# Kernel tuning notes

Measured on AMD Instinct MI355X. Metric: run time of the kernel, lower is better.

The kernel has to match this reference:

```python
import jax, jax.numpy as jnp
import numpy as np

N = 50000      # nodes
E = 800000     # edges (before self-loops)
F_IN = 128     # raw node feature dim
D = 500        # GCN_in_dim = gcn_dim = h_mlp_dim
T = 200000     # number of triplets


def setup_inputs() -> dict:
    key = jax.random.key(0)
    ks = jax.random.split(key, 13)
    s = 0.05
    return {
        "feats": jax.random.normal(ks[0], (N, F_IN), jnp.float32),
        "W_aff": jax.random.normal(ks[1], (F_IN, D), jnp.float32) * s,
        "b_aff": jax.random.normal(ks[2], (D,), jnp.float32) * s,
        "W_gcn": jax.random.normal(ks[3], (D, D), jnp.float32) * s,
        "b_gcn": jax.random.normal(ks[4], (D,), jnp.float32) * s,
        "W_pred_in": jax.random.normal(ks[5], (2 * D, D), jnp.float32) * s,
        "b_pred_in": jax.random.normal(ks[6], (D,), jnp.float32) * s,
        "W_pred_out": jax.random.normal(ks[7], (D, 1), jnp.float32) * s,
        "b_pred_out": jax.random.normal(ks[8], (1,), jnp.float32) * s,
        "src": jax.random.randint(ks[9], (E,), 0, N),
        "dst": jax.random.randint(ks[10], (E,), 0, N),
        "triplets": jax.random.randint(ks[11], (T, 3), 0, N),
    }


def reference(feats, W_aff, b_aff, W_gcn, b_gcn, W_pred_in, b_pred_in,
              W_pred_out, b_pred_out, src, dst, triplets):
    n = feats.shape[0]
    # LinearAffine (use_pre_linearAffine=True)
    x = feats @ W_aff + b_aff                      # [N, D]

    # dgl.add_self_loop
    loop = jnp.arange(n)
    s_idx = jnp.concatenate([src, loop])
    d_idx = jnp.concatenate([dst, loop])

    # GraphConv, norm='both', no edge weights, activation=None
    ones = jnp.ones(s_idx.shape[0], jnp.float32)
    out_deg = jax.ops.segment_sum(ones, s_idx, num_segments=n)
    in_deg = jax.ops.segment_sum(ones, d_idx, num_segments=n)
    norm_src = jnp.where(out_deg > 0, jax.lax.rsqrt(out_deg), 0.0)  # [N]
    norm_dst = jnp.where(in_deg > 0, jax.lax.rsqrt(in_deg), 0.0)    # [N]

    xw = x @ W_gcn                                  # [N, D]
    msg = xw[s_idx] * norm_src[s_idx, None]         # [E+N, D] gather
    agg = jax.ops.segment_sum(msg, d_idx, num_segments=n)  # scatter-add
    embedding = agg * norm_dst[:, None] + b_gcn     # [N, D]

    # triplet gather + MLP_edge_predictor (layer_num=2: cat->Linear->Linear)
    s_feat = embedding[triplets[:, 0]]              # [T, D]
    o_feat = embedding[triplets[:, 2]]              # [T, D]
    t = jnp.concatenate([s_feat, o_feat], axis=-1) @ W_pred_in + b_pred_in
    weights = t @ W_pred_out + b_pred_out           # [T, 1]
    return (weights, embedding)
```

## Files before the change

kernel.cpp:

```cpp
#include <hip/hip_runtime.h>


typedef float f32x4 __attribute__((ext_vector_type(4)));
typedef short s16x8 __attribute__((ext_vector_type(8)));

__device__ __forceinline__ unsigned short f2bf(float f) {
    unsigned u = __float_as_uint(f);
    unsigned r = (u + 0x7FFFu + ((u >> 16) & 1u)) >> 16;
    return (unsigned short)r;
}

__device__ __forceinline__ void async_ld16(const void* g, void* lds) {
    __builtin_amdgcn_global_load_lds(
        (const __attribute__((address_space(1))) unsigned int*)g,
        (__attribute__((address_space(3))) unsigned int*)lds,
        16, 0, 0);
}

__global__ __launch_bounds__(256) void hist2_kernel(
    const int* __restrict__ src, const int* __restrict__ dst,
    int* __restrict__ bhist_src, int* __restrict__ bhist_dst, int E) {
    __shared__ int lhs[256], lhd[256];
    lhs[threadIdx.x] = 0;
    lhd[threadIdx.x] = 0;
    __syncthreads();
    const int stride = gridDim.x * blockDim.x;
    for (int e = blockIdx.x * blockDim.x + threadIdx.x; e < E; e += stride) {
        atomicAdd(&lhs[src[e] >> 8], 1);
        atomicAdd(&lhd[dst[e] >> 8], 1);
    }
    __syncthreads();
    int cs = lhs[threadIdx.x], cd = lhd[threadIdx.x];
    if (cs > 0) atomicAdd(&bhist_src[threadIdx.x], cs);
    if (cd > 0) atomicAdd(&bhist_dst[threadIdx.x], cd);
}

__global__ void bscan2_kernel(const int* __restrict__ bhist_src, const int* __restrict__ bhist_dst,
                              int* __restrict__ sbbase, int* __restrict__ sbcursor,
                              int* __restrict__ dbbase, int* __restrict__ dbcursor,
                              int nbuk, int E) {
    __shared__ int sv[256];
    const int tid = threadIdx.x;

    int c = (tid < nbuk) ? bhist_src[tid] : 0;
    sv[tid] = c;
    __syncthreads();
    for (int st = 1; st < 256; st <<= 1) {
        int t = (tid >= st) ? sv[tid - st] : 0;
        __syncthreads();
        sv[tid] += t;
        __syncthreads();
    }
    if (tid < nbuk) { int ex = sv[tid] - c; sbbase[tid] = ex; sbcursor[tid] = ex; }
    if (tid == 0) sbbase[nbuk] = E;
    __syncthreads();

    c = (tid < nbuk) ? bhist_dst[tid] : 0;
    sv[tid] = c;
    __syncthreads();
    for (int st = 1; st < 256; st <<= 1) {
        int t = (tid >= st) ? sv[tid - st] : 0;
        __syncthreads();
        sv[tid] += t;
        __syncthreads();
    }
    if (tid < nbuk) { int ex = sv[tid] - c; dbbase[tid] = ex; dbcursor[tid] = ex; }
    if (tid == 0) dbbase[nbuk] = E;
}

#define PCH 4096
__global__ __launch_bounds__(256) void partition_kernel(
    const int* __restrict__ src, const int* __restrict__ dst,
    int* __restrict__ bcursor, unsigned long long* __restrict__ pairs,
    int E, int nbuk) {
    __shared__ int lhist[256];
    __shared__ int lbase[256];
    __shared__ int gbase[256];
    __shared__ int scanv[256];
    __shared__ unsigned long long lpair[PCH];
    __shared__ unsigned char lbid[PCH];

    const int tid = threadIdx.x;
    const int c0 = blockIdx.x * PCH;
    int cnt = E - c0; if (cnt > PCH) cnt = PCH;

    lhist[tid] = 0;
    __syncthreads();

    int dv[16], sv[16], rk[16];
#pragma unroll
    for (int q = 0; q < 16; ++q) {
        int e = c0 + q * 256 + tid;
        if (e < E) {
            int d = dst[e];
            dv[q] = d;
            sv[q] = src[e];
            rk[q] = atomicAdd(&lhist[d >> 8], 1);
        } else {
            dv[q] = -1;
        }
    }
    __syncthreads();

    int c = lhist[tid];
    scanv[tid] = c;
    __syncthreads();
    for (int st = 1; st < 256; st <<= 1) {
        int t = (tid >= st) ? scanv[tid - st] : 0;
        __syncthreads();
        scanv[tid] += t;
        __syncthreads();
    }
    lbase[tid] = scanv[tid] - c;
    if (tid < nbuk && c > 0) gbase[tid] = atomicAdd(&bcursor[tid], c);
    __syncthreads();

#pragma unroll
    for (int q = 0; q < 16; ++q) {
        if (dv[q] >= 0) {
            int b = dv[q] >> 8;
            int slot = lbase[b] + rk[q];
            lpair[slot] = ((unsigned long long)(unsigned)dv[q] << 32) | (unsigned)sv[q];
            lbid[slot] = (unsigned char)b;
        }
    }
    __syncthreads();

    for (int i = tid; i < cnt; i += 256) {
        int b = lbid[i];
        pairs[(long)gbase[b] + (i - lbase[b])] = lpair[i];
    }
}

__global__ __launch_bounds__(256) void partition_src_kernel(
    const int* __restrict__ src, int* __restrict__ bcursor,
    int* __restrict__ ssorted, int E, int nbuk) {
    __shared__ int lhist[256];
    __shared__ int lbase[256];
    __shared__ int gbase[256];
    __shared__ int scanv[256];
    __shared__ int lval[PCH];
    __shared__ unsigned char lbid[PCH];

    const int tid = threadIdx.x;
    const int c0 = blockIdx.x * PCH;
    int cnt = E - c0; if (cnt > PCH) cnt = PCH;

    lhist[tid] = 0;
    __syncthreads();

    int sv[16], rk[16];
#pragma unroll
    for (int q = 0; q < 16; ++q) {
        int e = c0 + q * 256 + tid;
        if (e < E) {
            int s = src[e];
            sv[q] = s;
            rk[q] = atomicAdd(&lhist[s >> 8], 1);
        } else {
            sv[q] = -1;
        }
    }
    __syncthreads();

    int c = lhist[tid];
    scanv[tid] = c;
    __syncthreads();
    for (int st = 1; st < 256; st <<= 1) {
        int t = (tid >= st) ? scanv[tid - st] : 0;
        __syncthreads();
        scanv[tid] += t;
        __syncthreads();
    }
    lbase[tid] = scanv[tid] - c;
    if (tid < nbuk && c > 0) gbase[tid] = atomicAdd(&bcursor[tid], c);
    __syncthreads();

#pragma unroll
    for (int q = 0; q < 16; ++q) {
        if (sv[q] >= 0) {
            int b = sv[q] >> 8;
            int slot = lbase[b] + rk[q];
            lval[slot] = sv[q];
            lbid[slot] = (unsigned char)b;
        }
    }
    __syncthreads();

    for (int i = tid; i < cnt; i += 256) {
        int b = lbid[i];
        ssorted[(long)gbase[b] + (i - lbase[b])] = lval[i];
    }
}

__global__ __launch_bounds__(256) void bucket_csr_kernel(
    const unsigned long long* __restrict__ pairs, const int* __restrict__ bbase,
    int* __restrict__ row_ptr, float* __restrict__ ndv,
    int* __restrict__ csr_src, int N) {
    __shared__ int hist[256];
    __shared__ int scanv[256];
    __shared__ int lcur[256];
    const int tid = threadIdx.x;
    const int b = blockIdx.x;
    const int e0 = bbase[b], e1 = bbase[b + 1];

    hist[tid] = 0;
    __syncthreads();
    for (int e = e0 + tid; e < e1; e += 256) {
        int d = (int)(pairs[e] >> 32);
        atomicAdd(&hist[d & 255], 1);
    }
    __syncthreads();

    int c = hist[tid];
    scanv[tid] = c;
    __syncthreads();
    for (int st = 1; st < 256; st <<= 1) {
        int t = (tid >= st) ? scanv[tid - st] : 0;
        __syncthreads();
        scanv[tid] += t;
        __syncthreads();
    }
    int excl = scanv[tid] - c;
    int node = b * 256 + tid;
    if (node < N) {
        row_ptr[node] = e0 + excl;
        ndv[node] = rsqrtf((float)(c + 1));
    }
    if (node == N) row_ptr[N] = e0 + excl;
    lcur[tid] = excl;
    __syncthreads();

    for (int e = e0 + tid; e < e1; e += 256) {
        unsigned long long pr = pairs[e];
        int d = (int)(pr >> 32);
        int r = atomicAdd(&lcur[d & 255], 1);
        csr_src[e0 + r] = (int)(pr & 0xFFFFFFFFu);
    }
}

__global__ __launch_bounds__(256) void bucket_ns_kernel(
    const int* __restrict__ ssorted, const int* __restrict__ sbbase,
    float* __restrict__ ns, int N) {
    __shared__ int hist[256];
    const int tid = threadIdx.x;
    const int b = blockIdx.x;
    const int e0 = sbbase[b], e1 = sbbase[b + 1];
    hist[tid] = 0;
    __syncthreads();
    for (int e = e0 + tid; e < e1; e += 256) atomicAdd(&hist[ssorted[e] & 255], 1);
    __syncthreads();
    int node = b * 256 + tid;
    if (node < N) ns[node] = rsqrtf((float)(hist[tid] + 1));
}

__global__ __launch_bounds__(256) void bcomb_part_kernel(
    const float* __restrict__ b_aff, const float* __restrict__ W_gcn,
    float* __restrict__ part, int D, int PD) {
    int n = blockIdx.x * blockDim.x + threadIdx.x;
    int c = blockIdx.y;
    if (n >= PD) return;
    float s = 0.f;
    if (n < D) {
        int k0 = c * 8;
        int k1 = k0 + 8; if (k1 > D) k1 = D;
        for (int k = k0; k < k1; ++k) s = fmaf(b_aff[k], W_gcn[(long)k * D + n], s);
    }
    part[(long)c * PD + n] = s;
}

__global__ void vcomb_kernel(const float* __restrict__ Win, const float* __restrict__ wout,
                             float* __restrict__ v, int D, int K2) {
    int k = blockIdx.x * (blockDim.x >> 6) + (threadIdx.x >> 6);
    int lane = threadIdx.x & 63;
    if (k >= K2) return;
    float s = 0.f;
    for (int c = lane; c < D; c += 64) s = fmaf(Win[(long)k * D + c], wout[c], s);
#pragma unroll
    for (int m = 32; m > 0; m >>= 1) s += __shfl_down(s, m);
    if (lane == 0) v[k] = s;
}

__global__ void bias_dot_kernel(const float* __restrict__ b_in, const float* __restrict__ w_out,
                                const float* __restrict__ b_out, float* __restrict__ bias_dot, int D) {
    __shared__ float sm[256];
    float s = 0.f;
    for (int c = threadIdx.x; c < D; c += 256) s = fmaf(b_in[c], w_out[c], s);
    sm[threadIdx.x] = s;
    __syncthreads();
    for (int st = 128; st > 0; st >>= 1) {
        if (threadIdx.x < st) sm[threadIdx.x] += sm[threadIdx.x + st];
        __syncthreads();
    }
    if (threadIdx.x == 0) bias_dot[0] = sm[0] + b_out[0];
}

__global__ void pad_kernel(const float* __restrict__ part, const float* __restrict__ b_gcn,
                           const float* __restrict__ v, float* __restrict__ bcp,
                           float* __restrict__ bgp, float* __restrict__ v1p,
                           float* __restrict__ v2p, int D, int PD, int NC) {
    int i = blockIdx.x * blockDim.x + threadIdx.x;
    if (i < PD) {
        float s = 0.f;
        for (int c = 0; c < NC; ++c) s += part[(long)c * PD + i];
        bcp[i] = s;
        bgp[i] = (i < D) ? b_gcn[i] : 0.f;
        v1p[i] = (i < D) ? v[i] : 0.f;
        v2p[i] = (i < D) ? v[D + i] : 0.f;
    }
}

__global__ __launch_bounds__(256) void sgemm_kernel(const float* __restrict__ A, int lda,
                                                    const float* __restrict__ B, int ldb,
                                                    float* __restrict__ C, int ldc,
                                                    int M, int N, int K) {
    __shared__ __align__(16) float As[16][68];
    __shared__ __align__(16) float Bs[16][68];
    const int tid = threadIdx.x;
    const int tx = tid & 15, ty = tid >> 4;
    const int row0 = blockIdx.x * 64;
    const int col0 = blockIdx.y * 64;

    const int a_row = tid >> 2;
    const int a_k   = (tid & 3) * 4;
    const int b_k   = tid >> 4;
    const int b_c   = (tid & 15) * 4;

    float acc[4][4] = {};

    for (int k0 = 0; k0 < K; k0 += 16) {
        float4 av = make_float4(0.f, 0.f, 0.f, 0.f);
        {
            int gr = row0 + a_row;
            int gk = k0 + a_k;
            if (gr < M) {
                if (gk + 3 < K) {
                    av = *reinterpret_cast<const float4*>(&A[(long)gr * lda + gk]);
                } else {
                    float t0 = (gk + 0 < K) ? A[(long)gr * lda + gk + 0] : 0.f;
                    float t1 = (gk + 1 < K) ? A[(long)gr * lda + gk + 1] : 0.f;
                    float t2 = (gk + 2 < K) ? A[(long)gr * lda + gk + 2] : 0.f;
                    float t3 = (gk + 3 < K) ? A[(long)gr * lda + gk + 3] : 0.f;
                    av = make_float4(t0, t1, t2, t3);
                }
            }
        }
        float4 bv = make_float4(0.f, 0.f, 0.f, 0.f);
        {
            int gk = k0 + b_k;
            int gc = col0 + b_c;
            if (gk < K) {
                if (gc + 3 < N) {
                    bv = *reinterpret_cast<const float4*>(&B[(long)gk * ldb + gc]);
                } else {
                    float t0 = (gc + 0 < N) ? B[(long)gk * ldb + gc + 0] : 0.f;
                    float t1 = (gc + 1 < N) ? B[(long)gk * ldb + gc + 1] : 0.f;
                    float t2 = (gc + 2 < N) ? B[(long)gk * ldb + gc + 2] : 0.f;
                    float t3 = (gc + 3 < N) ? B[(long)gk * ldb + gc + 3] : 0.f;
                    bv = make_float4(t0, t1, t2, t3);
                }
            }
        }
        __syncthreads();
        As[a_k + 0][a_row] = av.x;
        As[a_k + 1][a_row] = av.y;
        As[a_k + 2][a_row] = av.z;
        As[a_k + 3][a_row] = av.w;
        *reinterpret_cast<float4*>(&Bs[b_k][b_c]) = bv;
        __syncthreads();

#pragma unroll
        for (int k = 0; k < 16; ++k) {
            const float4 a = *reinterpret_cast<const float4*>(&As[k][ty * 4]);
            const float4 b = *reinterpret_cast<const float4*>(&Bs[k][tx * 4]);
            const float avv[4] = {a.x, a.y, a.z, a.w};
            const float bvv[4] = {b.x, b.y, b.z, b.w};
#pragma unroll
            for (int i = 0; i < 4; ++i)
#pragma unroll
                for (int j = 0; j < 4; ++j)
                    acc[i][j] = fmaf(avv[i], bvv[j], acc[i][j]);
        }
    }

#pragma unroll
    for (int i = 0; i < 4; ++i) {
        int r = row0 + ty * 4 + i;
        if (r >= M) continue;
#pragma unroll
        for (int j = 0; j < 4; ++j) {
            int c = col0 + tx * 4 + j;
            if (c < N) C[(long)r * ldc + c] = acc[i][j];
        }
    }
}

__global__ void conv_feats_kernel(const float* __restrict__ feats, const float* __restrict__ ns,
                                  unsigned short* __restrict__ fs16, int N) {
    int idx = blockIdx.x * blockDim.x + threadIdx.x;
    if (idx >= N * 16) return;
    int node = idx >> 4;
    int c = (idx & 15) * 8;
    float s = ns[node];
    const float* p = feats + (long)node * 128 + c;
    float4 a = *reinterpret_cast<const float4*>(p);
    float4 b = *reinterpret_cast<const float4*>(p + 4);
    uint4 o;
    o.x = (unsigned)f2bf(a.x * s) | ((unsigned)f2bf(a.y * s) << 16);
    o.y = (unsigned)f2bf(a.z * s) | ((unsigned)f2bf(a.w * s) << 16);
    o.z = (unsigned)f2bf(b.x * s) | ((unsigned)f2bf(b.y * s) << 16);
    o.w = (unsigned)f2bf(b.z * s) | ((unsigned)f2bf(b.w * s) << 16);
    *reinterpret_cast<uint4*>(fs16 + (long)node * 128 + c) = o;
}

__global__ void conv_Bt_kernel(const float* __restrict__ Wc, unsigned short* __restrict__ Bt,
                               int D, int PD) {
    int idx = blockIdx.x * blockDim.x + threadIdx.x;
    if (idx >= PD * 16) return;
    int n = idx >> 4;
    int k8 = (idx & 15) * 8;
    uint4 o = make_uint4(0, 0, 0, 0);
    if (n < D) {
        unsigned short t[8];
#pragma unroll
        for (int q = 0; q < 8; ++q) t[q] = f2bf(Wc[(long)(k8 + q) * D + n]);
        o.x = (unsigned)t[0] | ((unsigned)t[1] << 16);
        o.y = (unsigned)t[2] | ((unsigned)t[3] << 16);
        o.z = (unsigned)t[4] | ((unsigned)t[5] << 16);
        o.w = (unsigned)t[6] | ((unsigned)t[7] << 16);
    }
    *reinterpret_cast<uint4*>(Bt + (long)n * 128 + k8) = o;
}

__global__ __launch_bounds__(256) void gather_feats_kernel(
    const unsigned short* __restrict__ fs16, const int* __restrict__ csr_src,
    const int* __restrict__ row_ptr, const float* __restrict__ ns,
    unsigned short* __restrict__ g16, float* __restrict__ h, int N) {
    int d = blockIdx.x * 4 + (threadIdx.x >> 6);
    int lane = threadIdx.x & 63;
    if (d >= N) return;

    unsigned su = *reinterpret_cast<const unsigned*>(fs16 + (long)d * 128 + lane * 2);
    float a0 = __uint_as_float(su << 16);
    float a1 = __uint_as_float(su & 0xFFFF0000u);
    float hacc = 0.f;

    const int beg = row_ptr[d], end = row_ptr[d + 1];
    for (int j0 = beg; j0 < end; j0 += 64) {
        int cnt = end - j0;
        if (cnt > 64) cnt = 64;
        int s = (lane < cnt) ? csr_src[j0 + lane] : 0;
        if (lane < cnt) hacc += ns[s];
        int k = 0;
        for (; k + 4 <= cnt; k += 4) {
            int s0 = __shfl(s, k);
            int s1 = __shfl(s, k + 1);
            int s2 = __shfl(s, k + 2);
            int s3 = __shfl(s, k + 3);
            unsigned v0 = *reinterpret_cast<const unsigned*>(fs16 + (long)s0 * 128 + lane * 2);
            unsigned v1 = *reinterpret_cast<const unsigned*>(fs16 + (long)s1 * 128 + lane * 2);
            unsigned v2 = *reinterpret_cast<const unsigned*>(fs16 + (long)s2 * 128 + lane * 2);
            unsigned v3 = *reinterpret_cast<const unsigned*>(fs16 + (long)s3 * 128 + lane * 2);
            a0 += __uint_as_float(v0 << 16); a1 += __uint_as_float(v0 & 0xFFFF0000u);
            a0 += __uint_as_float(v1 << 16); a1 += __uint_as_float(v1 & 0xFFFF0000u);
            a0 += __uint_as_float(v2 << 16); a1 += __uint_as_float(v2 & 0xFFFF0000u);
            a0 += __uint_as_float(v3 << 16); a1 += __uint_as_float(v3 & 0xFFFF0000u);
        }
        for (; k < cnt; ++k) {
            int sk = __shfl(s, k);
            unsigned v = *reinterpret_cast<const unsigned*>(fs16 + (long)sk * 128 + lane * 2);
            a0 += __uint_as_float(v << 16);
            a1 += __uint_as_float(v & 0xFFFF0000u);
        }
    }
#pragma unroll
    for (int m = 32; m > 0; m >>= 1) hacc += __shfl_xor(hacc, m);
    if (lane == 0) h[d] = hacc + ns[d];
    unsigned o = (unsigned)f2bf(a0) | ((unsigned)f2bf(a1) << 16);
    *reinterpret_cast<unsigned*>(g16 + (long)d * 128 + lane * 2) = o;
}

__global__ __launch_bounds__(256) void gcn_gemm_kernel(
    const unsigned short* __restrict__ g16, const unsigned short* __restrict__ Bt,
    const float* __restrict__ h, const float* __restrict__ nd,
    const float* __restrict__ bcp, const float* __restrict__ bgp,
    const float* __restrict__ v1p, const float* __restrict__ v2p,
    float* __restrict__ emb, float* __restrict__ u1, float* __restrict__ u2,
    int M, int D) {

    __shared__ __align__(16) unsigned short As[128 * 32];
    __shared__ __align__(16) unsigned short Bs[128 * 32];

    const int tid  = threadIdx.x;
    const int w    = tid >> 6;
    const int lane = tid & 63;
    const int row0 = blockIdx.x * 128;
    const int col0 = blockIdx.y * 128;

    const int r0   = 2 * w * 16 + (lane >> 2);
    const int r1   = (2 * w + 1) * 16 + (lane >> 2);
    const int slot = lane & 3;
    const int c0   = slot ^ ((r0 >> 1) & 3);
    const int c1   = slot ^ ((r1 >> 1) & 3);

    const unsigned short* pA0 = g16 + (long)(row0 + r0) * 128 + c0 * 8;
    const unsigned short* pA1 = g16 + (long)(row0 + r1) * 128 + c1 * 8;
    const unsigned short* pB0 = Bt + (long)(col0 + r0) * 128 + c0 * 8;
    const unsigned short* pB1 = Bt + (long)(col0 + r1) * 128 + c1 * 8;

    unsigned short* dA0 = As + 2 * w * 512;
    unsigned short* dA1 = As + (2 * w + 1) * 512;
    unsigned short* dB0 = Bs + 2 * w * 512;
    unsigned short* dB1 = Bs + (2 * w + 1) * 512;

    const int wrow = (w & 1) * 64;
    const int wcol = (w >> 1) * 64;
    const int lm = lane & 15, q = lane >> 4;
    const s16x8* pa[4];
    const s16x8* pb[4];
#pragma unroll
    for (int i = 0; i < 4; ++i) {
        int r = wrow + i * 16 + lm;
        int cs = q ^ ((r >> 1) & 3);
        pa[i] = reinterpret_cast<const s16x8*>(As + r * 32 + cs * 8);
        int n = wcol + i * 16 + lm;
        int cs2 = q ^ ((n >> 1) & 3);
        pb[i] = reinterpret_cast<const s16x8*>(Bs + n * 32 + cs2 * 8);
    }

    f32x4 acc[4][4];
#pragma unroll
    for (int i = 0; i < 4; ++i)
#pragma unroll
        for (int j = 0; j < 4; ++j) acc[i][j] = (f32x4)0.f;

    for (int k0 = 0; k0 < 128; k0 += 32) {
        async_ld16(pA0 + k0, dA0);
        async_ld16(pA1 + k0, dA1);
        async_ld16(pB0 + k0, dB0);
        async_ld16(pB1 + k0, dB1);
        __syncthreads();

        s16x8 af[4], bf[4];
#pragma unroll
        for (int i = 0; i < 4; ++i) { af[i] = *pa[i]; bf[i] = *pb[i]; }
#pragma unroll
        for (int i = 0; i < 4; ++i)
#pragma unroll
            for (int j = 0; j < 4; ++j)
                acc[i][j] = __builtin_amdgcn_mfma_f32_16x16x32_bf16(af[i], bf[j], acc[i][j], 0, 0, 0);
        __syncthreads();
    }

    float bcv[4], bgv[4], w1[4], w2[4];
    int colv[4];
#pragma unroll
    for (int j = 0; j < 4; ++j) {
        int c = col0 + wcol + j * 16 + lm;
        colv[j] = c;
        bcv[j] = bcp[c];
        bgv[j] = bgp[c];
        w1[j] = v1p[c];
        w2[j] = v2p[c];
    }

#pragma unroll
    for (int i = 0; i < 4; ++i) {
        float p1[4], p2[4];
#pragma unroll
        for (int reg = 0; reg < 4; ++reg) {
            int row = row0 + wrow + i * 16 + q * 4 + reg;
            float hb = h[row];
            float sc = nd[row];
            float s1 = 0.f, s2 = 0.f;
#pragma unroll
            for (int j = 0; j < 4; ++j) {
                float o = fmaf(sc, acc[i][j][reg] + hb * bcv[j], bgv[j]);
                if (row < M && colv[j] < D) emb[(long)row * D + colv[j]] = o;
                s1 = fmaf(o, w1[j], s1);
                s2 = fmaf(o, w2[j], s2);
            }
            p1[reg] = s1;
            p2[reg] = s2;
        }
#pragma unroll
        for (int mask = 1; mask < 16; mask <<= 1)
#pragma unroll
            for (int reg = 0; reg < 4; ++reg) {
                p1[reg] += __shfl_xor(p1[reg], mask);
                p2[reg] += __shfl_xor(p2[reg], mask);
            }
        if (lm == 0) {
#pragma unroll
            for (int reg = 0; reg < 4; ++reg) {
                int row = row0 + wrow + i * 16 + q * 4 + reg;
                if (row < M) {
                    atomicAdd(&u1[row], p1[reg]);
                    atomicAdd(&u2[row], p2[reg]);
                }
            }
        }
    }
}

__global__ void weights_kernel(const int* __restrict__ trip, const float* __restrict__ u1,
                               const float* __restrict__ u2, const float* __restrict__ bdot,
                               float* __restrict__ w, int T) {
    int r = blockIdx.x * blockDim.x + threadIdx.x;
    if (r < T) {
        int s = trip[(long)r * 3 + 0];
        int o = trip[(long)r * 3 + 2];
        w[r] = u1[s] + u2[o] + bdot[0];
    }
}


extern "C" void kernel_launch(void* const* d_in, const int* in_sizes, int n_in,
                              void* d_out, int out_size, void* d_ws, size_t ws_size,
                              hipStream_t stream) {
    const float* feats      = (const float*)d_in[0];
    const float* W_aff      = (const float*)d_in[1];
    const float* b_aff      = (const float*)d_in[2];
    const float* W_gcn      = (const float*)d_in[3];
    const float* b_gcn      = (const float*)d_in[4];
    const float* W_pred_in  = (const float*)d_in[5];
    const float* b_pred_in  = (const float*)d_in[6];
    const float* W_pred_out = (const float*)d_in[7];
    const float* b_pred_out = (const float*)d_in[8];
    const int*   src        = (const int*)d_in[9];
    const int*   dst        = (const int*)d_in[10];
    const int*   trip       = (const int*)d_in[11];

    const int D = in_sizes[2];
    const int F = in_sizes[1] / D;
    const int N = in_sizes[0] / F;
    const int E = in_sizes[9];
    const int T = in_sizes[11] / 3;

    const int PD = 512;
    const int GX = (N + 127) / 128;
    const int Mpad = GX * 128;
    const int NC = (D + 7) / 8;
    const int NBUK = (N >> 8) + 1;

    float* weights = (float*)d_out;
    float* emb     = (float*)d_out + T;

    char* p = (char*)d_ws;
    unsigned short* fs16 = (unsigned short*)p;  p += (size_t)N * 128 * 2;
    unsigned short* g16  = (unsigned short*)p;  p += (size_t)Mpad * 128 * 2;
    unsigned long long* pairs = (unsigned long long*)p; p += (size_t)E * 8;
    int* ssorted = (int*)p;  p += (size_t)E * 4;
    unsigned short* Bt   = (unsigned short*)p;  p += (size_t)PD * 128 * 2;
    float* Wc   = (float*)p;  p += (size_t)F * D * 4;
    float* bparts = (float*)p;  p += (size_t)64 * PD * 4;
    float* bcp  = (float*)p;  p += PD * 4;
    float* bgp  = (float*)p;  p += PD * 4;
    float* v1p  = (float*)p;  p += PD * 4;
    float* v2p  = (float*)p;  p += PD * 4;
    float* v    = (float*)p;  p += 1024 * 4;
    float* bdot = (float*)p;  p += 16;
    float* ns   = (float*)p;  p += (size_t)N * 4;
    float* nd   = (float*)p;  p += (size_t)N * 4;
    float* h    = (float*)p;  p += (size_t)Mpad * 4;
    float* u1   = (float*)p;  p += (size_t)N * 4;
    float* u2   = (float*)p;  p += (size_t)N * 4;
    int* bhist_src = (int*)p;  p += 256 * 4;
    int* bhist_dst = (int*)p;  p += 256 * 4;
    int* sbbase   = (int*)p;  p += 260 * 4;
    int* sbcursor = (int*)p;  p += 256 * 4;
    int* dbbase   = (int*)p;  p += 260 * 4;
    int* dbcursor = (int*)p;  p += 256 * 4;
    int* row_ptr = (int*)p;  p += (size_t)(N + 1) * 4;
    int* csr_src = (int*)p;  p += (size_t)E * 4;

    hipMemsetAsync(bhist_src, 0, 512 * 4, stream);
    hipMemsetAsync(u1, 0, 2 * (size_t)N * sizeof(float), stream);
    hipMemsetAsync(g16 + (size_t)N * 128, 0, (size_t)(Mpad - N) * 128 * 2, stream);
    hipMemsetAsync(h + N, 0, (size_t)(Mpad - N) * 4, stream);

    hist2_kernel<<<256, 256, 0, stream>>>(src, dst, bhist_src, bhist_dst, E);
    bscan2_kernel<<<1, 256, 0, stream>>>(bhist_src, bhist_dst, sbbase, sbcursor,
                                         dbbase, dbcursor, NBUK, E);
    partition_kernel<<<(E + PCH - 1) / PCH, 256, 0, stream>>>(src, dst, dbcursor, pairs, E, NBUK);
    partition_src_kernel<<<(E + PCH - 1) / PCH, 256, 0, stream>>>(src, sbcursor, ssorted, E, NBUK);
    bucket_csr_kernel<<<NBUK, 256, 0, stream>>>(pairs, dbbase, row_ptr, nd, csr_src, N);
    bucket_ns_kernel<<<NBUK, 256, 0, stream>>>(ssorted, sbbase, ns, N);

    vcomb_kernel<<<(2 * D + 3) / 4, 256, 0, stream>>>(W_pred_in, W_pred_out, v, D, 2 * D);
    bias_dot_kernel<<<1, 256, 0, stream>>>(b_pred_in, W_pred_out, b_pred_out, bdot, D);

    {
        dim3 grid((F + 63) / 64, (D + 63) / 64);
        sgemm_kernel<<<grid, 256, 0, stream>>>(W_aff, D, W_gcn, D, Wc, D, F, D, D);
    }
    {
        dim3 grid((PD + 255) / 256, NC);
        bcomb_part_kernel<<<grid, 256, 0, stream>>>(b_aff, W_gcn, bparts, D, PD);
    }
    pad_kernel<<<(PD + 255) / 256, 256, 0, stream>>>(bparts, b_gcn, v, bcp, bgp, v1p, v2p, D, PD, NC);
    conv_Bt_kernel<<<(PD * 16 + 255) / 256, 256, 0, stream>>>(Wc, Bt, D, PD);

    conv_feats_kernel<<<(N * 16 + 255) / 256, 256, 0, stream>>>(feats, ns, fs16, N);

    gather_feats_kernel<<<(N + 3) / 4, 256, 0, stream>>>(fs16, csr_src, row_ptr, ns, g16, h, N);

    {
        dim3 grid(GX, PD / 128);
        gcn_gemm_kernel<<<grid, 256, 0, stream>>>(g16, Bt, h, nd, bcp, bgp, v1p, v2p,
                                                  emb, u1, u2, N, D);
    }

    weights_kernel<<<(T + 255) / 256, 256, 0, stream>>>(trip, u1, u2, bdot, weights, T);
}
```

Before: 365.4 us.

## Fuse src/dst partition and bucket kernels; vectorize feature gather with 16B loads

Merges the dst and src partition passes into one kernel that reads src/dst once and reuses shared memory, and merges the CSR-build and source-degree kernels into one finalize kernel, which cuts launches and redundant global reads. The bf16 feature gather now has each group of 16 lanes load a full 256-byte row with uint4 loads, so four neighbours are processed per wave step, followed by a cross-group shuffle reduction. This trades more registers and shuffle reductions for fewer, wider memory transactions, and leaves three quarters of the lanes idle at store time.

```diff
diff --git a/kernel.cpp b/kernel.cpp
--- a/kernel.cpp
+++ b/kernel.cpp
@@ -69,9 +69,10 @@
 }
 
 #define PCH 4096
-__global__ __launch_bounds__(256) void partition_kernel(
+__global__ __launch_bounds__(256) void fused_partition_kernel(
     const int* __restrict__ src, const int* __restrict__ dst,
-    int* __restrict__ bcursor, unsigned long long* __restrict__ pairs,
+    int* __restrict__ dcursor, unsigned long long* __restrict__ pairs,
+    int* __restrict__ scursor, int* __restrict__ ssorted,
     int E, int nbuk) {
     __shared__ int lhist[256];
     __shared__ int lbase[256];
@@ -84,10 +85,10 @@
     const int c0 = blockIdx.x * PCH;
     int cnt = E - c0; if (cnt > PCH) cnt = PCH;
 
+    int dv[16], sv[16], rk[16];
+
     lhist[tid] = 0;
     __syncthreads();
-
-    int dv[16], sv[16], rk[16];
 #pragma unroll
     for (int q = 0; q < 16; ++q) {
         int e = c0 + q * 256 + tid;
@@ -98,6 +99,7 @@
             rk[q] = atomicAdd(&lhist[d >> 8], 1);
         } else {
             dv[q] = -1;
+            sv[q] = -1;
         }
     }
     __syncthreads();
@@ -112,7 +114,7 @@
         __syncthreads();
     }
     lbase[tid] = scanv[tid] - c;
-    if (tid < nbuk && c > 0) gbase[tid] = atomicAdd(&bcursor[tid], c);
+    if (tid < nbuk && c > 0) gbase[tid] = atomicAdd(&dcursor[tid], c);
     __syncthreads();
 
 #pragma unroll
@@ -130,40 +132,18 @@
         int b = lbid[i];
         pairs[(long)gbase[b] + (i - lbase[b])] = lpair[i];
     }
-}
-
-__global__ __launch_bounds__(256) void partition_src_kernel(
-    const int* __restrict__ src, int* __restrict__ bcursor,
-    int* __restrict__ ssorted, int E, int nbuk) {
-    __shared__ int lhist[256];
-    __shared__ int lbase[256];
-    __shared__ int gbase[256];
-    __shared__ int scanv[256];
-    __shared__ int lval[PCH];
-    __shared__ unsigned char lbid[PCH];
-
-    const int tid = threadIdx.x;
-    const int c0 = blockIdx.x * PCH;
-    int cnt = E - c0; if (cnt > PCH) cnt = PCH;
-
+    __syncthreads();
+
+    int* lval = (int*)lpair;
     lhist[tid] = 0;
     __syncthreads();
-
-    int sv[16], rk[16];
 #pragma unroll
     for (int q = 0; q < 16; ++q) {
-        int e = c0 + q * 256 + tid;
-        if (e < E) {
-            int s = src[e];
-            sv[q] = s;
-            rk[q] = atomicAdd(&lhist[s >> 8], 1);
-        } else {
-            sv[q] = -1;
-        }
-    }
-    __syncthreads();
-
-    int c = lhist[tid];
+        if (sv[q] >= 0) rk[q] = atomicAdd(&lhist[sv[q] >> 8], 1);
+    }
+    __syncthreads();
+
+    c = lhist[tid];
     scanv[tid] = c;
     __syncthreads();
     for (int st = 1; st < 256; st <<= 1) {
@@ -173,7 +153,7 @@
         __syncthreads();
     }
     lbase[tid] = scanv[tid] - c;
-    if (tid < nbuk && c > 0) gbase[tid] = atomicAdd(&bcursor[tid], c);
+    if (tid < nbuk && c > 0) gbase[tid] = atomicAdd(&scursor[tid], c);
     __syncthreads();
 
 #pragma unroll
@@ -193,17 +173,19 @@
     }
 }
 
-__global__ __launch_bounds__(256) void bucket_csr_kernel(
-    const unsigned long long* __restrict__ pairs, const int* __restrict__ bbase,
+__global__ __launch_bounds__(256) void bucket_finalize_kernel(
+    const unsigned long long* __restrict__ pairs, const int* __restrict__ dbbase,
+    const int* __restrict__ ssorted, const int* __restrict__ sbbase,
     int* __restrict__ row_ptr, float* __restrict__ ndv,
-    int* __restrict__ csr_src, int N) {
+    int* __restrict__ csr_src, float* __restrict__ ns, int N) {
     __shared__ int hist[256];
     __shared__ int scanv[256];
     __shared__ int lcur[256];
     const int tid = threadIdx.x;
     const int b = blockIdx.x;
-    const int e0 = bbase[b], e1 = bbase[b + 1];
-
+    const int node = b * 256 + tid;
+
+    const int e0 = dbbase[b], e1 = dbbase[b + 1];
     hist[tid] = 0;
     __syncthreads();
     for (int e = e0 + tid; e < e1; e += 256) {
@@ -222,7 +204,6 @@
         __syncthreads();
     }
     int excl = scanv[tid] - c;
-    int node = b * 256 + tid;
     if (node < N) {
         row_ptr[node] = e0 + excl;
         ndv[node] = rsqrtf((float)(c + 1));
@@ -237,20 +218,13 @@
         int r = atomicAdd(&lcur[d & 255], 1);
         csr_src[e0 + r] = (int)(pr & 0xFFFFFFFFu);
     }
-}
-
-__global__ __launch_bounds__(256) void bucket_ns_kernel(
-    const int* __restrict__ ssorted, const int* __restrict__ sbbase,
-    float* __restrict__ ns, int N) {
-    __shared__ int hist[256];
-    const int tid = threadIdx.x;
-    const int b = blockIdx.x;
-    const int e0 = sbbase[b], e1 = sbbase[b + 1];
+
+    __syncthreads();
     hist[tid] = 0;
     __syncthreads();
-    for (int e = e0 + tid; e < e1; e += 256) atomicAdd(&hist[ssorted[e] & 255], 1);
-    __syncthreads();
-    int node = b * 256 + tid;
+    const int s0 = sbbase[b], s1 = sbbase[b + 1];
+    for (int e = s0 + tid; e < s1; e += 256) atomicAdd(&hist[ssorted[e] & 255], 1);
+    __syncthreads();
     if (node < N) ns[node] = rsqrtf((float)(hist[tid] + 1));
 }
 
@@ -439,10 +413,10 @@
     int d = blockIdx.x * 4 + (threadIdx.x >> 6);
     int lane = threadIdx.x & 63;
     if (d >= N) return;
-
-    unsigned su = *reinterpret_cast<const unsigned*>(fs16 + (long)d * 128 + lane * 2);
-    float a0 = __uint_as_float(su << 16);
-    float a1 = __uint_as_float(su & 0xFFFF0000u);
+    const int g = lane >> 4;
+    const int fl = lane & 15;
+
+    float a[8] = {0.f, 0.f, 0.f, 0.f, 0.f, 0.f, 0.f, 0.f};
     float hacc = 0.f;
 
     const int beg = row_ptr[d], end = row_ptr[d + 1];
@@ -451,33 +425,47 @@
         if (cnt > 64) cnt = 64;
         int s = (lane < cnt) ? csr_src[j0 + lane] : 0;
         if (lane < cnt) hacc += ns[s];
-        int k = 0;
-        for (; k + 4 <= cnt; k += 4) {
-            int s0 = __shfl(s, k);
-            int s1 = __shfl(s, k + 1);
-            int s2 = __shfl(s, k + 2);
-            int s3 = __shfl(s, k + 3);
-            unsigned v0 = *reinterpret_cast<const unsigned*>(fs16 + (long)s0 * 128 + lane * 2);
-            unsigned v1 = *reinterpret_cast<const unsigned*>(fs16 + (long)s1 * 128 + lane * 2);
-            unsigned v2 = *reinterpret_cast<const unsigned*>(fs16 + (long)s2 * 128 + lane * 2);
-            unsigned v3 = *reinterpret_cast<const unsigned*>(fs16 + (long)s3 * 128 + lane * 2);
-            a0 += __uint_as_float(v0 << 16); a1 += __uint_as_float(v0 & 0xFFFF0000u);
-            a0 += __uint_as_float(v1 << 16); a1 += __uint_as_float(v1 & 0xFFFF0000u);
-            a0 += __uint_as_float(v2 << 16); a1 += __uint_as_float(v2 & 0xFFFF0000u);
-            a0 += __uint_as_float(v3 << 16); a1 += __uint_as_float(v3 & 0xFFFF0000u);
-        }
-        for (; k < cnt; ++k) {
-            int sk = __shfl(s, k);
-            unsigned v = *reinterpret_cast<const unsigned*>(fs16 + (long)sk * 128 + lane * 2);
-            a0 += __uint_as_float(v << 16);
-            a1 += __uint_as_float(v & 0xFFFF0000u);
-        }
+        for (int k = 0; k < cnt; k += 8) {
+            int k0 = k + g, k1 = k + 4 + g;
+            int i0 = __shfl(s, k0 & 63);
+            int i1 = __shfl(s, k1 & 63);
+            uint4 v0 = make_uint4(0u, 0u, 0u, 0u), v1 = make_uint4(0u, 0u, 0u, 0u);
+            if (k0 < cnt) v0 = *reinterpret_cast<const uint4*>(fs16 + (long)i0 * 128 + fl * 8);
+            if (k1 < cnt) v1 = *reinterpret_cast<const uint4*>(fs16 + (long)i1 * 128 + fl * 8);
+            a[0] += __uint_as_float(v0.x << 16); a[1] += __uint_as_float(v0.x & 0xFFFF0000u);
+            a[2] += __uint_as_float(v0.y << 16); a[3] += __uint_as_float(v0.y & 0xFFFF0000u);
+            a[4] += __uint_as_float(v0.z << 16); a[5] += __uint_as_float(v0.z & 0xFFFF0000u);
+            a[6] += __uint_as_float(v0.w << 16); a[7] += __uint_as_float(v0.w & 0xFFFF0000u);
+            a[0] += __uint_as_float(v1.x << 16); a[1] += __uint_as_float(v1.x & 0xFFFF0000u);
+            a[2] += __uint_as_float(v1.y << 16); a[3] += __uint_as_float(v1.y & 0xFFFF0000u);
+            a[4] += __uint_as_float(v1.z << 16); a[5] += __uint_as_float(v1.z & 0xFFFF0000u);
+            a[6] += __uint_as_float(v1.w << 16); a[7] += __uint_as_float(v1.w & 0xFFFF0000u);
+        }
+    }
+
+#pragma unroll
+    for (int r = 0; r < 8; ++r) {
+        a[r] += __shfl_xor(a[r], 16);
+        a[r] += __shfl_xor(a[r], 32);
+    }
+    {
+        uint4 sv4 = *reinterpret_cast<const uint4*>(fs16 + (long)d * 128 + fl * 8);
+        a[0] += __uint_as_float(sv4.x << 16); a[1] += __uint_as_float(sv4.x & 0xFFFF0000u);
+        a[2] += __uint_as_float(sv4.y << 16); a[3] += __uint_as_float(sv4.y & 0xFFFF0000u);
+        a[4] += __uint_as_float(sv4.z << 16); a[5] += __uint_as_float(sv4.z & 0xFFFF0000u);
+        a[6] += __uint_as_float(sv4.w << 16); a[7] += __uint_as_float(sv4.w & 0xFFFF0000u);
     }
 #pragma unroll
     for (int m = 32; m > 0; m >>= 1) hacc += __shfl_xor(hacc, m);
     if (lane == 0) h[d] = hacc + ns[d];
-    unsigned o = (unsigned)f2bf(a0) | ((unsigned)f2bf(a1) << 16);
-    *reinterpret_cast<unsigned*>(g16 + (long)d * 128 + lane * 2) = o;
+    if (lane < 16) {
+        uint4 o;
+        o.x = (unsigned)f2bf(a[0]) | ((unsigned)f2bf(a[1]) << 16);
+        o.y = (unsigned)f2bf(a[2]) | ((unsigned)f2bf(a[3]) << 16);
+        o.z = (unsigned)f2bf(a[4]) | ((unsigned)f2bf(a[5]) << 16);
+        o.w = (unsigned)f2bf(a[6]) | ((unsigned)f2bf(a[7]) << 16);
+        *reinterpret_cast<uint4*>(g16 + (long)d * 128 + fl * 8) = o;
+    }
 }
 
 __global__ __launch_bounds__(256) void gcn_gemm_kernel(
@@ -682,10 +670,10 @@
     hist2_kernel<<<256, 256, 0, stream>>>(src, dst, bhist_src, bhist_dst, E);
     bscan2_kernel<<<1, 256, 0, stream>>>(bhist_src, bhist_dst, sbbase, sbcursor,
                                          dbbase, dbcursor, NBUK, E);
-    partition_kernel<<<(E + PCH - 1) / PCH, 256, 0, stream>>>(src, dst, dbcursor, pairs, E, NBUK);
-    partition_src_kernel<<<(E + PCH - 1) / PCH, 256, 0, stream>>>(src, sbcursor, ssorted, E, NBUK);
-    bucket_csr_kernel<<<NBUK, 256, 0, stream>>>(pairs, dbbase, row_ptr, nd, csr_src, N);
-    bucket_ns_kernel<<<NBUK, 256, 0, stream>>>(ssorted, sbbase, ns, N);
+    fused_partition_kernel<<<(E + PCH - 1) / PCH, 256, 0, stream>>>(
+        src, dst, dbcursor, pairs, sbcursor, ssorted, E, NBUK);
+    bucket_finalize_kernel<<<NBUK, 256, 0, stream>>>(pairs, dbbase, ssorted, sbbase,
+                                                     row_ptr, nd, csr_src, ns, N);
 
     vcomb_kernel<<<(2 * D + 3) / 4, 256, 0, stream>>>(W_pred_in, W_pred_out, v, D, 2 * D);
     bias_dot_kernel<<<1, 256, 0, stream>>>(b_pred_in, W_pred_out, b_pred_out, bdot, D);
```

Result: faster. 354.9 us (-2.9%).
